# Kernel optimization log

Hardware: AMD Instinct MI355X
Metric: run time of the kernel (lower is better)

## Reference

```python
import jax, jax.numpy as jnp
import numpy as np

B, T, N, DG = 4, 24, 2048, 64
E, H, W, P, NH = 128, 64, 64, 8, 4
HD = E // NH
HP, WP = H // P, W // P
NP = HP * WP
SCALE = float(np.sqrt(HD))


def _mlp(x, w1, b1, w2, b2):
    return jax.nn.relu(x @ w1 + b1) @ w2 + b2


def _interp_linear(x, out_len):
    # x: (B, L, C); linear interpolation along L to out_len, align_corners=False (PyTorch semantics)
    L = x.shape[1]
    src = jnp.maximum((jnp.arange(out_len, dtype=jnp.float32) + 0.5) * (L / out_len) - 0.5, 0.0)
    i0 = jnp.floor(src).astype(jnp.int32)
    lam = (src - i0.astype(jnp.float32))[None, :, None]
    i1 = jnp.minimum(i0 + 1, L - 1)
    return x[:, i0] * (1.0 - lam) + x[:, i1] * lam


def _cross_attn(Q, K, V, qw, qb, kw, kb, vw, vb, ow, ob):
    b, ql, _ = Q.shape
    kl = K.shape[1]
    q = (Q @ qw + qb).reshape(b, ql, NH, HD).transpose(0, 2, 1, 3)
    k = (K @ kw + kb).reshape(b, kl, NH, HD).transpose(0, 2, 1, 3)
    v = (V @ vw + vb).reshape(b, kl, NH, HD).transpose(0, 2, 1, 3)
    s = jnp.einsum('bhqd,bhkd->bhqk', q, k) / SCALE
    a = jax.nn.softmax(s, axis=-1)
    o = jnp.einsum('bhqk,bhkd->bhqd', a, v).transpose(0, 2, 1, 3).reshape(b, ql, E)
    o = o @ ow + ob
    # permute -> F.interpolate(size=k_len, mode='linear') -> permute back
    return _interp_linear(o, kl)


def _forward(graph_features, grid_features, graph_time_indices, grid_time_indices,
             gek_w1, gek_b1, gek_w2, gek_b2, gev_w1, gev_b1, gev_w2, gev_b2,
             rk_w1, rk_b1, rk_w2, rk_b2, rv_w1, rv_b1, rv_w2, rv_b2,
             te_w1, te_b1, te_w2, te_b2, pe_w, pe_b, up_w, up_b,
             ag_q_w, ag_q_b, ag_k_w, ag_k_b, ag_v_w, ag_v_b, ag_o_w, ag_o_b,
             ar_q_w, ar_q_b, ar_k_w, ar_k_b, ar_v_w, ar_v_b, ar_o_w, ar_o_b):
    # time embedding (query), q_len = T
    te = _mlp(graph_time_indices[:, :, None], te_w1, te_b1, te_w2, te_b2)  # (B, T, E)
    # graph branch
    gf = graph_features.reshape(B, T * N, DG)
    gk = _mlp(gf, gek_w1, gek_b1, gek_w2, gek_b2)
    gv = _mlp(gf, gev_w1, gev_b1, gev_w2, gev_b2)
    g_out = _cross_attn(te, gk, gv, ag_q_w, ag_q_b, ag_k_w, ag_k_b, ag_v_w, ag_v_b, ag_o_w, ag_o_b)
    g_out = g_out.reshape(B, T, N, E)
    # grid branch: non-overlapping patch conv (kernel=stride=P) as einsum
    xp = grid_features.reshape(B * T, E, HP, P, WP, P)
    patches = jnp.einsum('bchpwq,ocpq->bhwo', xp, pe_w) + pe_b  # (BT, HP, WP, E)
    patches = patches.reshape(B, T * NP, E)
    rk = _mlp(patches, rk_w1, rk_b1, rk_w2, rk_b2)
    rv = _mlp(patches, rv_w1, rv_b1, rv_w2, rv_b2)
    r_out = _cross_attn(te, rk, rv, ar_q_w, ar_q_b, ar_k_w, ar_k_b, ar_v_w, ar_v_b, ar_o_w, ar_o_b)  # (B, T*NP, E)
    r = r_out.reshape(B * T, HP, WP, E)
    # ConvTranspose2d with kernel=stride=P: each pixel expands to a PxP block
    up = jnp.einsum('bijc,copq->boipjq', r, up_w).reshape(B * T, E, H, W) + up_b[None, :, None, None]
    return g_out, up.reshape(B, T, E, H, W)


def setup_inputs():
    key = jax.random.key(0)
    ks = iter(jax.random.split(key, 64))
    def mk(shape):
        return jax.random.normal(next(ks), shape, dtype=jnp.float32) * 0.02
    d = {}
    d['graph_features'] = jax.random.normal(next(ks), (B, T, N, DG), dtype=jnp.float32)
    d['grid_features'] = jax.random.normal(next(ks), (B, T, E, H, W), dtype=jnp.float32)
    d['graph_time_indices'] = jax.random.uniform(next(ks), (B, T), dtype=jnp.float32)
    d['grid_time_indices'] = jax.random.uniform(next(ks), (B, T), dtype=jnp.float32)
    for pfx, din in (('gek', DG), ('gev', DG), ('rk', E), ('rv', E), ('te', 1)):
        d[pfx + '_w1'] = mk((din, E)); d[pfx + '_b1'] = jnp.zeros((E,), jnp.float32)
        d[pfx + '_w2'] = mk((E, E)); d[pfx + '_b2'] = jnp.zeros((E,), jnp.float32)
    d['pe_w'] = mk((E, E, P, P)); d['pe_b'] = jnp.zeros((E,), jnp.float32)
    d['up_w'] = mk((E, E, P, P)); d['up_b'] = jnp.zeros((E,), jnp.float32)
    for pfx in ('ag', 'ar'):
        for nm in ('q', 'k', 'v', 'o'):
            d[pfx + '_' + nm + '_w'] = mk((E, E)); d[pfx + '_' + nm + '_b'] = jnp.zeros((E,), jnp.float32)
    return d


def reference(graph_features, grid_features, graph_time_indices, grid_time_indices,
              gek_w1, gek_b1, gek_w2, gek_b2, gev_w1, gev_b1, gev_w2, gev_b2,
              rk_w1, rk_b1, rk_w2, rk_b2, rv_w1, rv_b1, rv_w2, rv_b2,
              te_w1, te_b1, te_w2, te_b2, pe_w, pe_b, up_w, up_b,
              ag_q_w, ag_q_b, ag_k_w, ag_k_b, ag_v_w, ag_v_b, ag_o_w, ag_o_b,
              ar_q_w, ar_q_b, ar_k_w, ar_k_b, ar_v_w, ar_v_b, ar_o_w, ar_o_b):
    return _forward(graph_features, grid_features, graph_time_indices, grid_time_indices,
                    gek_w1, gek_b1, gek_w2, gek_b2, gev_w1, gev_b1, gev_w2, gev_b2,
                    rk_w1, rk_b1, rk_w2, rk_b2, rv_w1, rv_b1, rv_w2, rv_b2,
                    te_w1, te_b1, te_w2, te_b2, pe_w, pe_b, up_w, up_b,
                    ag_q_w, ag_q_b, ag_k_w, ag_k_b, ag_v_w, ag_v_b, ag_o_w, ag_o_b,
                    ar_q_w, ar_q_b, ar_k_w, ar_k_b, ar_v_w, ar_v_b, ar_o_w, ar_o_b)
```

## Files before the change

### kernel.cpp

```cpp
#include <hip/hip_runtime.h>


typedef unsigned short u16;
using bf8 = __attribute__((ext_vector_type(8))) short;
using f4v = __attribute__((ext_vector_type(4))) float;
#define MFMA16(a, b, c) __builtin_amdgcn_mfma_f32_16x16x32_bf16(a, b, c, 0, 0, 0)

constexpr float INV_SCALE = 0.17677669529663687f;

__device__ __forceinline__ u16 f2bf(float f) {
  unsigned u = __float_as_uint(f);
  u += 0x7FFFu + ((u >> 16) & 1u);
  return (u16)(u >> 16);
}
__device__ __forceinline__ unsigned pk2(float a, float b) {
  return (unsigned)f2bf(a) | ((unsigned)f2bf(b) << 16);
}
__device__ __forceinline__ float bflo(unsigned v) { return __uint_as_float(v << 16); }
__device__ __forceinline__ float bfhi(unsigned v) { return __uint_as_float(v & 0xffff0000u); }


__global__ __launch_bounds__(128) void k_pre1(
    const float* gk_w1, const float* gv_w1, const float* rk_w1, const float* rv_w1,
    u16* W1c_g, u16* W1c_r,
    const float* pe_w, u16* peB,
    const float* tidx, const float* te_w1, const float* te_b1,
    const float* te_w2, const float* te_b2,
    const float* wg, const float* bg, const float* wr, const float* br,
    float* qg, float* qr,
    const float* A0, const float* Ab0, const float* B0, const float* Bb0, float* O0, float* Ob0,
    const float* A1, const float* Ab1, const float* B1, const float* Bb1, float* O1, float* Ob1,
    const float* A2, const float* Ab2, const float* B2, const float* Bb2, float* O2, float* Ob2,
    const float* A3, const float* Ab3, const float* B3, const float* Bb3, float* O3, float* Ob3) {
  int x = blockIdx.x, e = threadIdx.x;
  __shared__ float sh[256];
  if (x < 512) {
    int c = x & 255, brn = x >> 8;
    int DIN = brn ? 128 : 64;
    if (e < DIN) {
      const float* src = brn ? (c < 128 ? rk_w1 : rv_w1) : (c < 128 ? gk_w1 : gv_w1);
      u16* dst = brn ? W1c_r : W1c_g;
      dst[c * DIN + e] = f2bf(src[e * 128 + (c & 127)]);
    }
  } else if (x < 1536) {
    int i = ((x - 512) * 128 + e) * 8;
    float4 v0 = *(const float4*)(pe_w + i);
    float4 v1 = *(const float4*)(pe_w + i + 4);
    uint4 o; o.x = pk2(v0.x, v0.y); o.y = pk2(v0.z, v0.w);
    o.z = pk2(v1.x, v1.y); o.w = pk2(v1.z, v1.w);
    *(uint4*)&peB[i] = o;
  } else if (x < 1632) {
    int row = x - 1536;
    float tv = tidx[row];
    sh[e] = fmaxf(tv * te_w1[e] + te_b1[e], 0.f);
    __syncthreads();
    float a = te_b2[e];
    for (int j = 0; j < 128; ++j) a += sh[j] * te_w2[j * 128 + e];
    sh[128 + e] = a;
    __syncthreads();
    float ag = bg[e], ar = br[e];
    for (int j = 0; j < 128; ++j) {
      float xx = sh[128 + j];
      ag += xx * wg[j * 128 + e];
      ar += xx * wr[j * 128 + e];
    }
    qg[row * 128 + e] = ag;
    qr[row * 128 + e] = ar;
  } else {
    int sub = x - 1632;
    int task = sub / 129, j = sub % 129;
    const float *A, *Ab, *Bm, *Bb; float *O, *Ob;
    switch (task) {
      case 0: A=A0; Ab=Ab0; Bm=B0; Bb=Bb0; O=O0; Ob=Ob0; break;
      case 1: A=A1; Ab=Ab1; Bm=B1; Bb=Bb1; O=O1; Ob=Ob1; break;
      case 2: A=A2; Ab=Ab2; Bm=B2; Bb=Bb2; O=O2; Ob=Ob2; break;
      default:A=A3; Ab=Ab3; Bm=B3; Bb=Bb3; O=O3; Ob=Ob3; break;
    }
    sh[e] = (j < 128) ? A[j * 128 + e] : Ab[e];
    __syncthreads();
    float acc = (j < 128) ? 0.f : Bb[e];
    for (int m = 0; m < 128; ++m) acc += sh[m] * Bm[m * 128 + e];
    if (j < 128) O[j * 128 + e] = acc; else Ob[e] = acc;
  }
}


__global__ __launch_bounds__(128) void k_wvopk(
    const float* Wv_g, const float* bv_g, const float* ow_g, const float* ob_g, float* Wvo_g, float* bvo_g,
    const float* Wv_r, const float* bv_r, const float* ow_r, const float* ob_r, float* Wvo_r, float* bvo_r,
    const float* Wk_g, const float* bk_g, const float* q_g, u16* PkT_g, float* ck_g,
    const float* Wk_r, const float* bk_r, const float* q_r, u16* PkT_r, float* ck_r) {
  int j = blockIdx.x, e = threadIdx.x;
  if (blockIdx.y < 8) {
    int br = blockIdx.y >> 2, h = blockIdx.y & 3;
    const float* Wv = br ? Wv_r : Wv_g;  const float* bv = br ? bv_r : bv_g;
    const float* ow = br ? ow_r : ow_g;  const float* ob = br ? ob_r : ob_g;
    float* Wvo = br ? Wvo_r : Wvo_g;     float* bvo = br ? bvo_r : bvo_g;
    if (j < 128) {
      __shared__ float wrow[32];
      if (e < 32) wrow[e] = Wv[j * 128 + h * 32 + e];
      __syncthreads();
      float acc = 0.f;
      for (int d = 0; d < 32; ++d) acc += wrow[d] * ow[(h * 32 + d) * 128 + e];
      Wvo[(h * 128 + j) * 128 + e] = acc;
    } else if (h == 0) {
      __shared__ float bbv[128];
      bbv[e] = bv[e];
      __syncthreads();
      float acc = ob[e];
      for (int m = 0; m < 128; ++m) acc += bbv[m] * ow[m * 128 + e];
      bvo[e] = acc;
    }
  } else {
    int y = blockIdx.y - 8;
    int br = y >> 2, b = y & 3;
    int hq = e;
    if (hq >= 96) return;
    const float* Wk = br ? Wk_r : Wk_g;  const float* bk = br ? bk_r : bk_g;
    const float* q  = br ? q_r  : q_g;
    u16* PkT = br ? PkT_r : PkT_g;       float* ck = br ? ck_r : ck_g;
    int h = hq / 24, t = hq % 24;
    const float* qrow = q + (b * 24 + t) * 128 + h * 32;
    if (j < 128) {
      const float* wrow = Wk + j * 128 + h * 32;
      float acc = 0.f;
      for (int d = 0; d < 32; ++d) acc += wrow[d] * qrow[d];
      PkT[((size_t)b * 96 + hq) * 136 + j] = f2bf(acc * INV_SCALE);
    } else {
      float acc = 0.f;
      for (int d = 0; d < 32; ++d) acc += bk[h * 32 + d] * qrow[d];
      ck[b * 96 + hq] = acc * INV_SCALE;
    }
  }
}


template <int DIN, int NRED, bool INBF>
__device__ __forceinline__ void flash_body(char* smem,
    const void* __restrict__ Xv, const float* __restrict__ redbias, size_t rstride,
    const u16* __restrict__ W1c, const float* __restrict__ b1k, const float* __restrict__ b1v,
    const u16* __restrict__ PkT, const float* __restrict__ ck,
    u16* __restrict__ accP, float* __restrict__ lP,
    int KL, int kpb, int chunk, int b, int nchunk) {
  constexpr int KS = DIN / 32;
  constexpr int PD = DIN + 8;
  constexpr int PH = 136, PV = 72, PP = 72;
  constexpr int NR = DIN / 16;
  constexpr int XTN = 64 * PD;
  u16* Xt   = (u16*)smem;
  u16* HB   = (u16*)(smem + 4 * XTN);
  u16* Pt   = (u16*)(smem + 4 * XTN + 18432);
  u16* Pk_s = (u16*)(smem + 4 * XTN + 18432 + 13824);
  float* lred = (float*)(smem + 4 * XTN + 18432 + 13824 + 26112);

  int t = threadIdx.x;
  int l = t & 63, w = t >> 6;
  int l16 = l & 15, l4 = l >> 4;

  size_t xbase = (size_t)b * KL * DIN + (size_t)chunk * kpb * DIN;

  {
    const unsigned* ps = (const unsigned*)(PkT + (size_t)b * 96 * 136);
    unsigned* pd = (unsigned*)Pk_s;
    for (int i = t; i < 96 * 136 / 2; i += 256) pd[i] = ps[i];
  }

  bf8 wkA[2][KS], wvB[2][KS];
#pragma unroll
  for (int m = 0; m < 2; ++m)
#pragma unroll
    for (int ks = 0; ks < KS; ++ks) {
      int hid = w * 32 + m * 16 + l16;
      wkA[m][ks] = *(const bf8*)(W1c + (size_t)hid * DIN + ks * 32 + l4 * 8);
      wvB[m][ks] = *(const bf8*)(W1c + (size_t)(128 + hid) * DIN + ks * 32 + l4 * 8);
    }
  float bkA[2][4], bvB[2], ckr[6];
#pragma unroll
  for (int m = 0; m < 2; ++m)
#pragma unroll
    for (int r = 0; r < 4; ++r) bkA[m][r] = b1k[w * 32 + m * 16 + l4 * 4 + r];
#pragma unroll
  for (int n = 0; n < 2; ++n) bvB[n] = b1v[w * 32 + n * 16 + l16];
#pragma unroll
  for (int n = 0; n < 6; ++n) ckr[n] = ck[b * 96 + n * 16 + l16];

  f4v accO[6][2];
#pragma unroll
  for (int m = 0; m < 6; ++m)
#pragma unroll
    for (int n = 0; n < 2; ++n) accO[m][n] = (f4v){0.f, 0.f, 0.f, 0.f};
  float lacc[6] = {0.f, 0.f, 0.f, 0.f, 0.f, 0.f};

  float4 xr[NR];
  auto load_tile = [&](int kt) {
#pragma unroll
    for (int r = 0; r < NR; ++r) {
      int idx = (r * 256 + t) * 4;
      if constexpr (!INBF) {
        const float* Xrow = (const float*)Xv + xbase + (size_t)kt * 64 * DIN;
        xr[r] = *(const float4*)(Xrow + idx);
      } else {
        const u16* Xrow = (const u16*)Xv + xbase + (size_t)kt * 64 * DIN;
        int din = idx % DIN;
        float4 a = *(const float4*)(redbias + din);
#pragma unroll
        for (int c = 0; c < NRED; ++c) {
          uint2 v = *(const uint2*)(Xrow + (size_t)c * rstride + idx);
          a.x += bflo(v.x); a.y += bfhi(v.x);
          a.z += bflo(v.y); a.w += bfhi(v.y);
        }
        xr[r] = a;
      }
    }
  };

  int ntile = kpb >> 6;
  load_tile(0);
  int buf = 0;
  for (int kt = 0; kt < ntile; ++kt) {
#pragma unroll
    for (int r = 0; r < NR; ++r) {
      int idx = (r * 256 + t) * 4;
      int key = idx / DIN, din = idx % DIN;
      uint2 o; o.x = pk2(xr[r].x, xr[r].y); o.y = pk2(xr[r].z, xr[r].w);
      *(uint2*)&Xt[buf * XTN + key * PD + din] = o;
    }
    if (kt + 1 < ntile) load_tile(kt + 1);
    __syncthreads();

    {
      f4v hk[2][4];
#pragma unroll
      for (int m = 0; m < 2; ++m)
#pragma unroll
        for (int n = 0; n < 4; ++n) hk[m][n] = (f4v){0.f, 0.f, 0.f, 0.f};
#pragma unroll
      for (int ks = 0; ks < KS; ++ks) {
        bf8 xf[4];
#pragma unroll
        for (int n = 0; n < 4; ++n)
          xf[n] = *(const bf8*)&Xt[buf * XTN + (n * 16 + l16) * PD + ks * 32 + l4 * 8];
#pragma unroll
        for (int m = 0; m < 2; ++m)
#pragma unroll
          for (int n = 0; n < 4; ++n) hk[m][n] = MFMA16(wkA[m][ks], xf[n], hk[m][n]);
      }
#pragma unroll
      for (int m = 0; m < 2; ++m)
#pragma unroll
        for (int n = 0; n < 4; ++n) {
          int key = n * 16 + l16;
          int hid0 = w * 32 + m * 16 + l4 * 4;
          float v0 = fmaxf(hk[m][n][0] + bkA[m][0], 0.f);
          float v1 = fmaxf(hk[m][n][1] + bkA[m][1], 0.f);
          float v2 = fmaxf(hk[m][n][2] + bkA[m][2], 0.f);
          float v3 = fmaxf(hk[m][n][3] + bkA[m][3], 0.f);
          uint2 o; o.x = pk2(v0, v1); o.y = pk2(v2, v3);
          *(uint2*)&HB[key * PH + hid0] = o;
        }
    }
    __syncthreads();

    {
      f4v sa[6];
#pragma unroll
      for (int n = 0; n < 6; ++n) sa[n] = (f4v){ckr[n], ckr[n], ckr[n], ckr[n]};
#pragma unroll
      for (int ks = 0; ks < 4; ++ks) {
        bf8 a = *(const bf8*)&HB[(w * 16 + l16) * PH + ks * 32 + l4 * 8];
#pragma unroll
        for (int n = 0; n < 6; ++n) {
          bf8 bp = *(const bf8*)&Pk_s[(n * 16 + l16) * 136 + ks * 32 + l4 * 8];
          sa[n] = MFMA16(a, bp, sa[n]);
        }
      }
#pragma unroll
      for (int n = 0; n < 6; ++n) {
        float e0 = __expf(sa[n][0]), e1 = __expf(sa[n][1]);
        float e2 = __expf(sa[n][2]), e3 = __expf(sa[n][3]);
        float ls = (e0 + e1) + (e2 + e3);
        ls += __shfl_xor(ls, 16);
        ls += __shfl_xor(ls, 32);
        lacc[n] += ls;
        uint2 o; o.x = pk2(e0, e1); o.y = pk2(e2, e3);
        *(uint2*)&Pt[(n * 16 + l16) * PP + w * 16 + l4 * 4] = o;
      }
    }
    __syncthreads();

    {
      f4v hv[4][2];
#pragma unroll
      for (int m = 0; m < 4; ++m)
#pragma unroll
        for (int n = 0; n < 2; ++n) hv[m][n] = (f4v){0.f, 0.f, 0.f, 0.f};
#pragma unroll
      for (int ks = 0; ks < KS; ++ks) {
        bf8 xa[4];
#pragma unroll
        for (int m = 0; m < 4; ++m)
          xa[m] = *(const bf8*)&Xt[buf * XTN + (m * 16 + l16) * PD + ks * 32 + l4 * 8];
#pragma unroll
        for (int m = 0; m < 4; ++m)
#pragma unroll
          for (int n = 0; n < 2; ++n) hv[m][n] = MFMA16(xa[m], wvB[n][ks], hv[m][n]);
      }
#pragma unroll
      for (int m = 0; m < 4; ++m)
#pragma unroll
        for (int n = 0; n < 2; ++n) {
          int d = w * 32 + n * 16 + l16;
          int key0 = m * 16 + l4 * 4;
          float v0 = fmaxf(hv[m][n][0] + bvB[n], 0.f);
          float v1 = fmaxf(hv[m][n][1] + bvB[n], 0.f);
          float v2 = fmaxf(hv[m][n][2] + bvB[n], 0.f);
          float v3 = fmaxf(hv[m][n][3] + bvB[n], 0.f);
          uint2 o; o.x = pk2(v0, v1); o.y = pk2(v2, v3);
          *(uint2*)&HB[d * PV + key0] = o;
        }
    }

#pragma unroll
    for (int ks = 0; ks < 2; ++ks) {
      bf8 pa[6];
#pragma unroll
      for (int m = 0; m < 6; ++m)
        pa[m] = *(const bf8*)&Pt[(m * 16 + l16) * PP + ks * 32 + l4 * 8];
#pragma unroll
      for (int n = 0; n < 2; ++n) {
        bf8 hb = *(const bf8*)&HB[(w * 32 + n * 16 + l16) * PV + ks * 32 + l4 * 8];
#pragma unroll
        for (int m = 0; m < 6; ++m) accO[m][n] = MFMA16(pa[m], hb, accO[m][n]);
      }
    }
    buf ^= 1;
  }

  u16* ap = accP + (size_t)(b * nchunk + chunk) * 96 * 128;
#pragma unroll
  for (int m = 0; m < 6; ++m)
#pragma unroll
    for (int n = 0; n < 2; ++n) {
      int d = w * 32 + n * 16 + l16;
#pragma unroll
      for (int r = 0; r < 4; ++r) {
        int hq = m * 16 + l4 * 4 + r;
        ap[hq * 128 + d] = f2bf(accO[m][n][r]);
      }
    }
  if (l4 == 0) {
#pragma unroll
    for (int n = 0; n < 6; ++n) lred[w * 96 + n * 16 + l16] = lacc[n];
  }
  __syncthreads();
  if (t < 96) {
    float s = lred[t] + lred[96 + t] + lred[192 + t] + lred[288 + t];
    lP[(size_t)(b * nchunk + chunk) * 96 + t] = s;
  }
}


__device__ __forceinline__ void patch_body(char* smem, int bt, int kc,
    const float* __restrict__ X, const u16* __restrict__ peB,
    u16* __restrict__ patchP) {
  u16* Xp = (u16*)smem;
  u16* Wt = (u16*)(smem + 17408);
  int t = threadIdx.x;
  int l = t & 63, w = t >> 6;
  int l16 = l & 15, l4 = l >> 4;
  const float* Xbt = X + (size_t)bt * 524288 + (size_t)kc * 65536;

  f4v acc[4][2];
#pragma unroll
  for (int m = 0; m < 4; ++m)
#pragma unroll
    for (int n = 0; n < 2; ++n) acc[m][n] = (f4v){0.f, 0.f, 0.f, 0.f};

  float4 xr[8];
  auto loadX = [&](int s) {
    const float* img = Xbt + (size_t)s * 8192;
#pragma unroll
    for (int r = 0; r < 8; ++r) xr[r] = *(const float4*)(img + (r * 256 + t) * 4);
  };
  loadX(0);

  for (int s = 0; s < 8; ++s) {
#pragma unroll
    for (int r = 0; r < 8; ++r) {
      int idx = (r * 256 + t) * 4;
      int cl = idx >> 12, off = idx & 4095;
      int h = off >> 6, w0 = off & 63;
      int patch = (h >> 3) * 8 + (w0 >> 3);
      int within = (h & 7) * 8 + (w0 & 7);
      uint2 o; o.x = pk2(xr[r].x, xr[r].y); o.y = pk2(xr[r].z, xr[r].w);
      *(uint2*)&Xp[patch * 136 + cl * 64 + within] = o;
    }
    {
      int colbase = kc * 1024 + s * 128;
#pragma unroll
      for (int r = 0; r < 8; ++r) {
        int idx = r * 256 + t;
        int co = idx >> 4, part = idx & 15;
        int slot = part ^ (co & 7);
        uint4 v = *(const uint4*)(peB + (size_t)co * 8192 + colbase + part * 8);
        *(uint4*)&Wt[co * 128 + slot * 8] = v;
      }
    }
    if (s < 7) loadX(s + 1);
    __syncthreads();
#pragma unroll
    for (int ks2 = 0; ks2 < 4; ++ks2) {
      bf8 af[4];
#pragma unroll
      for (int m = 0; m < 4; ++m)
        af[m] = *(const bf8*)&Xp[(m * 16 + l16) * 136 + ks2 * 32 + l4 * 8];
#pragma unroll
      for (int n = 0; n < 2; ++n) {
        int co = w * 32 + n * 16 + l16;
        int slot = (ks2 * 4 + l4) ^ (co & 7);
        bf8 bf_ = *(const bf8*)&Wt[co * 128 + slot * 8];
#pragma unroll
        for (int m = 0; m < 4; ++m) acc[m][n] = MFMA16(af[m], bf_, acc[m][n]);
      }
    }
    __syncthreads();
  }
  u16* outp = patchP + ((size_t)kc * 6144 + bt * 64) * 128;
#pragma unroll
  for (int m = 0; m < 4; ++m)
#pragma unroll
    for (int n = 0; n < 2; ++n) {
      int d = w * 32 + n * 16 + l16;
#pragma unroll
      for (int r = 0; r < 4; ++r) {
        int patch = m * 16 + l4 * 4 + r;
        outp[patch * 128 + d] = f2bf(acc[m][n][r]);
      }
    }
}


__device__ __forceinline__ void ogred_body(char* smem, int t, int b, int nc,
    const u16* __restrict__ accP, const float* __restrict__ lP,
    const float* __restrict__ Wvo, const float* __restrict__ bvo,
    float* __restrict__ og) {
  float* part = (float*)smem;
  float* invl = part + 2048;
  float* red  = part + 2052;
  int tid = threadIdx.x;
  int oct = tid & 15, h = (tid >> 4) & 3, cq = tid >> 6;
  int cn = nc >> 2;
  float a8[8];
#pragma unroll
  for (int k = 0; k < 8; ++k) a8[k] = 0.f;
  const u16* base = accP + ((size_t)(b * nc + cq * cn) * 96 + h * 24 + t) * 128 + oct * 8;
  for (int c = 0; c < cn; ++c) {
    uint4 v = *(const uint4*)(base + (size_t)c * 12288);
    a8[0] += bflo(v.x); a8[1] += bfhi(v.x);
    a8[2] += bflo(v.y); a8[3] += bfhi(v.y);
    a8[4] += bflo(v.z); a8[5] += bfhi(v.z);
    a8[6] += bflo(v.w); a8[7] += bfhi(v.w);
  }
#pragma unroll
  for (int k = 0; k < 8; ++k) part[cq * 512 + h * 128 + oct * 8 + k] = a8[k];
  if (tid < 64) {
    int hh = tid >> 4, c0 = tid & 15;
    float ls = 0.f;
    for (int c = c0; c < nc; c += 16) ls += lP[(size_t)(b * nc + c) * 96 + hh * 24 + t];
    ls += __shfl_xor(ls, 8); ls += __shfl_xor(ls, 4);
    ls += __shfl_xor(ls, 2); ls += __shfl_xor(ls, 1);
    if (c0 == 0) invl[hh] = 1.f / ls;
  }
  __syncthreads();
  for (int p = tid; p < 512; p += 256) {
    float s = (part[p] + part[512 + p]) + (part[1024 + p] + part[1536 + p]);
    part[p] = s * invl[p >> 7];
  }
  __syncthreads();
  {
    int e = tid & 127, jh = tid >> 7;
    float acc = jh ? 0.f : bvo[e];
    for (int h2 = 0; h2 < 4; ++h2) {
      const float* wv = Wvo + (size_t)(h2 * 128 + jh * 64) * 128 + e;
      const float* o = part + h2 * 128 + jh * 64;
#pragma unroll 4
      for (int j = 0; j < 64; ++j) acc += o[j] * wv[(size_t)j * 128];
    }
    red[tid] = acc;
  }
  __syncthreads();
  if (tid < 128) og[(b * 24 + t) * 128 + tid] = red[tid] + red[128 + tid];
}


__global__ __launch_bounds__(256, 2) void k_big1(
    const float* __restrict__ gf, const u16* __restrict__ W1c_g,
    const float* __restrict__ gek_b1, const float* __restrict__ gev_b1,
    const u16* __restrict__ PkT_g, const float* __restrict__ ck_g,
    u16* __restrict__ accP_g, float* __restrict__ lP_g,
    const float* __restrict__ gridf, const u16* __restrict__ peB,
    u16* __restrict__ patchP) {
  __shared__ __align__(16) char smem[78336];
  int x = blockIdx.x;
  int r5 = x % 5, q5 = x / 5;
  if (r5 < 2) {
    int fid = q5 * 2 + r5;
    flash_body<64, 1, false>(smem, gf, (const float*)nullptr, 0,
        W1c_g, gek_b1, gev_b1, PkT_g, ck_g, accP_g, lP_g,
        49152, 384, fid & 127, fid >> 7, 128);
  } else {
    int pid = q5 * 3 + (r5 - 2);
    patch_body(smem, pid % 96, pid / 96, gridf, peB, patchP);
  }
}


__global__ __launch_bounds__(256, 2) void k_big2(
    const u16* __restrict__ accP_g, const float* __restrict__ lP_g,
    const float* __restrict__ Wvo_g, const float* __restrict__ bvo_g,
    float* __restrict__ og_g,
    const u16* __restrict__ patchP, const float* __restrict__ pe_b,
    const u16* __restrict__ W1c_r,
    const float* __restrict__ rk_b1, const float* __restrict__ rv_b1,
    const u16* __restrict__ PkT_r, const float* __restrict__ ck_r,
    u16* __restrict__ accP_r, float* __restrict__ lP_r) {
  __shared__ __align__(16) char smem[94720];
  int x = blockIdx.x;
  int id = x >> 1;
  if (x & 1) {
    flash_body<128, 8, true>(smem, patchP, pe_b, 786432,
        W1c_r, rk_b1, rv_b1, PkT_r, ck_r, accP_r, lP_r,
        1536, 64, id % 24, id / 24, 24);
  } else {
    ogred_body(smem, id % 24, id / 24, 128, accP_g, lP_g, Wvo_g, bvo_g, og_g);
  }
}


__global__ __launch_bounds__(256) void k_ogr(
    const u16* __restrict__ accP_r, const float* __restrict__ lP_r,
    const float* __restrict__ Wvo_r, const float* __restrict__ bvo_r,
    float* __restrict__ og_r) {
  __shared__ __align__(16) char smem[9232];
  int x = blockIdx.x;
  ogred_body(smem, x % 24, x / 24, 24, accP_r, lP_r, Wvo_r, bvo_r, og_r);
}


__global__ __launch_bounds__(256) void k_writers(const float* __restrict__ og_r,
    const float* __restrict__ up_w, const float* __restrict__ up_b,
    float* __restrict__ outu,
    const float* __restrict__ og_g, float* __restrict__ outg) {
  __shared__ float og_s[24 * 128];
  __shared__ float upw_s[128 * 64];
  __shared__ float U_s[24 * 64];
  int x = blockIdx.x;
  if (x < 512) {
    int b = x >> 7, o = x & 127;
    int tid = threadIdx.x;
    for (int i = tid; i < 24 * 128 / 4; i += 256)
      ((float4*)og_s)[i] = ((const float4*)(og_r + b * 3072))[i];
    for (int i = tid; i < 128 * 64 / 4; i += 256) {
      int c = i >> 4, pq4 = i & 15;
      ((float4*)upw_s)[i] = *(const float4*)(up_w + (size_t)c * 8192 + o * 64 + pq4 * 4);
    }
    __syncthreads();
    float bias = up_b[o];
    int pq = tid & 63, tg = tid >> 6;
    float acc[6] = {0.f, 0.f, 0.f, 0.f, 0.f, 0.f};
    for (int c = 0; c < 128; c += 4) {
      float w0 = upw_s[c * 64 + pq], w1 = upw_s[(c + 1) * 64 + pq];
      float w2 = upw_s[(c + 2) * 64 + pq], w3 = upw_s[(c + 3) * 64 + pq];
#pragma unroll
      for (int r = 0; r < 6; ++r) {
        float4 g = *(const float4*)&og_s[(tg * 6 + r) * 128 + c];
        acc[r] += g.x * w0 + g.y * w1 + g.z * w2 + g.w * w3;
      }
    }
#pragma unroll
    for (int r = 0; r < 6; ++r) U_s[(tg * 6 + r) * 64 + pq] = acc[r] + bias;
    __syncthreads();
    for (int i4 = tid; i4 < 24 * 1024; i4 += 256) {
      int i = i4 * 4;
      int t = i >> 12, hw = i & 4095;
      int h = hw >> 6, w0 = hw & 63;
      int ii = h >> 3, p = h & 7, j = w0 >> 3, q0 = w0 & 7;
      int n = t * 64 + ii * 8 + j;
      float src = fmaxf((n + 0.5f) * (1.f / 64.f) - 0.5f, 0.f);
      int t0 = (int)src; float lam = src - (float)t0; int t1 = min(t0 + 1, 23);
      float4 a = *(const float4*)&U_s[t0 * 64 + p * 8 + q0];
      float4 c4 = *(const float4*)&U_s[t1 * 64 + p * 8 + q0];
      float4 r;
      r.x = a.x + lam * (c4.x - a.x); r.y = a.y + lam * (c4.y - a.y);
      r.z = a.z + lam * (c4.z - a.z); r.w = a.w + lam * (c4.w - a.w);
      *(float4*)&outu[((size_t)(b * 24 + t) * 128 + o) * 4096 + hw] = r;
    }
  } else {
    int vx = x - 512;
    int b = vx >> 10;
    const float* ogb = og_g + b * 3072;
    float* ob = outg + (size_t)b * 6291456;
    for (int i4 = (vx & 1023) * 256 + threadIdx.x; i4 < 1572864; i4 += 1024 * 256) {
      int i = i4 * 4;
      int n = i >> 7, e = i & 127;
      float src = fmaxf((n + 0.5f) * (1.f / 2048.f) - 0.5f, 0.f);
      int t0 = (int)src; float lam = src - (float)t0; int t1 = min(t0 + 1, 23);
      float4 a = *(const float4*)&ogb[t0 * 128 + e];
      float4 c = *(const float4*)&ogb[t1 * 128 + e];
      float4 o;
      o.x = a.x + lam * (c.x - a.x); o.y = a.y + lam * (c.y - a.y);
      o.z = a.z + lam * (c.z - a.z); o.w = a.w + lam * (c.w - a.w);
      *(float4*)&ob[i] = o;
    }
  }
}


extern "C" void kernel_launch(void* const* d_in, const int* in_sizes, int n_in,
                              void* d_out, int out_size, void* d_ws, size_t ws_size,
                              hipStream_t stream) {
  (void)in_sizes; (void)n_in; (void)out_size; (void)ws_size;
  const float* gf    = (const float*)d_in[0];
  const float* gridf = (const float*)d_in[1];
  const float* gti   = (const float*)d_in[2];
  const float* gek_w1 = (const float*)d_in[4],  *gek_b1 = (const float*)d_in[5];
  const float* gek_w2 = (const float*)d_in[6],  *gek_b2 = (const float*)d_in[7];
  const float* gev_w1 = (const float*)d_in[8],  *gev_b1 = (const float*)d_in[9];
  const float* gev_w2 = (const float*)d_in[10], *gev_b2 = (const float*)d_in[11];
  const float* rk_w1  = (const float*)d_in[12], *rk_b1  = (const float*)d_in[13];
  const float* rk_w2  = (const float*)d_in[14], *rk_b2  = (const float*)d_in[15];
  const float* rv_w1  = (const float*)d_in[16], *rv_b1  = (const float*)d_in[17];
  const float* rv_w2  = (const float*)d_in[18], *rv_b2  = (const float*)d_in[19];
  const float* te_w1  = (const float*)d_in[20], *te_b1  = (const float*)d_in[21];
  const float* te_w2  = (const float*)d_in[22], *te_b2  = (const float*)d_in[23];
  const float* pe_w   = (const float*)d_in[24], *pe_b   = (const float*)d_in[25];
  const float* up_w   = (const float*)d_in[26], *up_b   = (const float*)d_in[27];
  const float* ag_q_w = (const float*)d_in[28], *ag_q_b = (const float*)d_in[29];
  const float* ag_k_w = (const float*)d_in[30], *ag_k_b = (const float*)d_in[31];
  const float* ag_v_w = (const float*)d_in[32], *ag_v_b = (const float*)d_in[33];
  const float* ag_o_w = (const float*)d_in[34], *ag_o_b = (const float*)d_in[35];
  const float* ar_q_w = (const float*)d_in[36], *ar_q_b = (const float*)d_in[37];
  const float* ar_k_w = (const float*)d_in[38], *ar_k_b = (const float*)d_in[39];
  const float* ar_v_w = (const float*)d_in[40], *ar_v_b = (const float*)d_in[41];
  const float* ar_o_w = (const float*)d_in[42], *ar_o_b = (const float*)d_in[43];

  float* out = (float*)d_out;
  float* ws = (float*)d_ws;
  size_t off = 0;
  auto A = [&](size_t n) { float* p = ws + off; off += n; return p; };
  float* q_g   = A(12288);   float* q_r   = A(12288);
  float* Wk_g  = A(16384);   float* bk_g  = A(128);
  float* Wv_g  = A(16384);   float* bv_g  = A(128);
  float* Wk_r  = A(16384);   float* bk_r  = A(128);
  float* Wv_r  = A(16384);   float* bv_r  = A(128);
  float* Wvo_g = A(65536);   float* bvo_g = A(128);
  float* Wvo_r = A(65536);   float* bvo_r = A(128);
  float* ck_g  = A(384);     float* ck_r  = A(384);
  u16*   PkT_g = (u16*)A(26112);
  u16*   PkT_r = (u16*)A(26112);
  u16*   W1c_g = (u16*)A(8192);
  u16*   W1c_r = (u16*)A(16384);
  u16*   peB   = (u16*)A(524288);
  float* lP_g  = A(49152);   float* lP_r  = A(9216);
  float* og_g  = A(12288);   float* og_r  = A(12288);
  u16*   accP_g = (u16*)A(3145728);
  u16*   patchP = (u16*)A(3145728);
  u16*   accP_r = (u16*)A(589824);

  k_pre1<<<2148, 128, 0, stream>>>(
      gek_w1, gev_w1, rk_w1, rv_w1, W1c_g, W1c_r,
      pe_w, peB,
      gti, te_w1, te_b1, te_w2, te_b2, ag_q_w, ag_q_b, ar_q_w, ar_q_b, q_g, q_r,
      gek_w2, gek_b2, ag_k_w, ag_k_b, Wk_g, bk_g,
      gev_w2, gev_b2, ag_v_w, ag_v_b, Wv_g, bv_g,
      rk_w2,  rk_b2,  ar_k_w, ar_k_b, Wk_r, bk_r,
      rv_w2,  rv_b2,  ar_v_w, ar_v_b, Wv_r, bv_r);
  k_wvopk<<<dim3(129, 16), 128, 0, stream>>>(
      Wv_g, bv_g, ag_o_w, ag_o_b, Wvo_g, bvo_g,
      Wv_r, bv_r, ar_o_w, ar_o_b, Wvo_r, bvo_r,
      Wk_g, bk_g, q_g, PkT_g, ck_g,
      Wk_r, bk_r, q_r, PkT_r, ck_r);

  k_big1<<<1280, 256, 0, stream>>>(
      gf, W1c_g, gek_b1, gev_b1, PkT_g, ck_g, accP_g, lP_g,
      gridf, peB, patchP);
  k_big2<<<192, 256, 0, stream>>>(
      accP_g, lP_g, Wvo_g, bvo_g, og_g,
      patchP, pe_b, W1c_r, rk_b1, rv_b1, PkT_r, ck_r, accP_r, lP_r);
  k_ogr<<<96, 256, 0, stream>>>(accP_r, lP_r, Wvo_r, bvo_r, og_r);
  k_writers<<<4608, 256, 0, stream>>>(og_r, up_w, up_b, out + 25165824, og_g, out);
}
```

Before: 213.5 us.

## Rebalance flash split counts and move graph broadcast writer alongside grid reduction

Reduces the number of key-chunk splits in both flash-attention stages: 32 instead of 128 for the graph branch and 8 instead of 24 for the grid branch. This shrinks the partial-accumulator buffers and the split-reduction work in ogred. Block interleaving in k_big1/k_big2 becomes contiguous ranges. The graph-output broadcast writer now shares a launch with the grid split reduction, overlapping it with the reduction instead of waiting behind it, and the up-projection writer becomes its own kernel. Fewer, longer flash blocks reduce merge overhead but may lower occupancy and load balance across CUs.

```diff
diff --git a/kernel.cpp b/kernel.cpp
--- a/kernel.cpp
+++ b/kernel.cpp
@@ -502,14 +502,12 @@
     u16* __restrict__ patchP) {
   __shared__ __align__(16) char smem[78336];
   int x = blockIdx.x;
-  int r5 = x % 5, q5 = x / 5;
-  if (r5 < 2) {
-    int fid = q5 * 2 + r5;
+  if (x < 128) {
     flash_body<64, 1, false>(smem, gf, (const float*)nullptr, 0,
         W1c_g, gek_b1, gev_b1, PkT_g, ck_g, accP_g, lP_g,
-        49152, 384, fid & 127, fid >> 7, 128);
+        49152, 1536, x & 31, x >> 5, 32);
   } else {
-    int pid = q5 * 3 + (r5 - 2);
+    int pid = x - 128;
     patch_body(smem, pid % 96, pid / 96, gridf, peB, patchP);
   }
 }
@@ -526,77 +524,28 @@
     u16* __restrict__ accP_r, float* __restrict__ lP_r) {
   __shared__ __align__(16) char smem[94720];
   int x = blockIdx.x;
-  int id = x >> 1;
-  if (x & 1) {
+  if (x < 96) {
+    ogred_body(smem, x % 24, x / 24, 32, accP_g, lP_g, Wvo_g, bvo_g, og_g);
+  } else {
+    int fid = x - 96;
     flash_body<128, 8, true>(smem, patchP, pe_b, 786432,
         W1c_r, rk_b1, rv_b1, PkT_r, ck_r, accP_r, lP_r,
-        1536, 64, id % 24, id / 24, 24);
-  } else {
-    ogred_body(smem, id % 24, id / 24, 128, accP_g, lP_g, Wvo_g, bvo_g, og_g);
-  }
-}
-
-
-__global__ __launch_bounds__(256) void k_ogr(
+        1536, 192, fid & 7, fid >> 3, 8);
+  }
+}
+
+
+__global__ __launch_bounds__(256) void k_big3(
     const u16* __restrict__ accP_r, const float* __restrict__ lP_r,
     const float* __restrict__ Wvo_r, const float* __restrict__ bvo_r,
-    float* __restrict__ og_r) {
+    float* __restrict__ og_r,
+    const float* __restrict__ og_g, float* __restrict__ outg) {
   __shared__ __align__(16) char smem[9232];
   int x = blockIdx.x;
-  ogred_body(smem, x % 24, x / 24, 24, accP_r, lP_r, Wvo_r, bvo_r, og_r);
-}
-
-
-__global__ __launch_bounds__(256) void k_writers(const float* __restrict__ og_r,
-    const float* __restrict__ up_w, const float* __restrict__ up_b,
-    float* __restrict__ outu,
-    const float* __restrict__ og_g, float* __restrict__ outg) {
-  __shared__ float og_s[24 * 128];
-  __shared__ float upw_s[128 * 64];
-  __shared__ float U_s[24 * 64];
-  int x = blockIdx.x;
-  if (x < 512) {
-    int b = x >> 7, o = x & 127;
-    int tid = threadIdx.x;
-    for (int i = tid; i < 24 * 128 / 4; i += 256)
-      ((float4*)og_s)[i] = ((const float4*)(og_r + b * 3072))[i];
-    for (int i = tid; i < 128 * 64 / 4; i += 256) {
-      int c = i >> 4, pq4 = i & 15;
-      ((float4*)upw_s)[i] = *(const float4*)(up_w + (size_t)c * 8192 + o * 64 + pq4 * 4);
-    }
-    __syncthreads();
-    float bias = up_b[o];
-    int pq = tid & 63, tg = tid >> 6;
-    float acc[6] = {0.f, 0.f, 0.f, 0.f, 0.f, 0.f};
-    for (int c = 0; c < 128; c += 4) {
-      float w0 = upw_s[c * 64 + pq], w1 = upw_s[(c + 1) * 64 + pq];
-      float w2 = upw_s[(c + 2) * 64 + pq], w3 = upw_s[(c + 3) * 64 + pq];
-#pragma unroll
-      for (int r = 0; r < 6; ++r) {
-        float4 g = *(const float4*)&og_s[(tg * 6 + r) * 128 + c];
-        acc[r] += g.x * w0 + g.y * w1 + g.z * w2 + g.w * w3;
-      }
-    }
-#pragma unroll
-    for (int r = 0; r < 6; ++r) U_s[(tg * 6 + r) * 64 + pq] = acc[r] + bias;
-    __syncthreads();
-    for (int i4 = tid; i4 < 24 * 1024; i4 += 256) {
-      int i = i4 * 4;
-      int t = i >> 12, hw = i & 4095;
-      int h = hw >> 6, w0 = hw & 63;
-      int ii = h >> 3, p = h & 7, j = w0 >> 3, q0 = w0 & 7;
-      int n = t * 64 + ii * 8 + j;
-      float src = fmaxf((n + 0.5f) * (1.f / 64.f) - 0.5f, 0.f);
-      int t0 = (int)src; float lam = src - (float)t0; int t1 = min(t0 + 1, 23);
-      float4 a = *(const float4*)&U_s[t0 * 64 + p * 8 + q0];
-      float4 c4 = *(const float4*)&U_s[t1 * 64 + p * 8 + q0];
-      float4 r;
-      r.x = a.x + lam * (c4.x - a.x); r.y = a.y + lam * (c4.y - a.y);
-      r.z = a.z + lam * (c4.z - a.z); r.w = a.w + lam * (c4.w - a.w);
-      *(float4*)&outu[((size_t)(b * 24 + t) * 128 + o) * 4096 + hw] = r;
-    }
+  if (x < 96) {
+    ogred_body(smem, x % 24, x / 24, 8, accP_r, lP_r, Wvo_r, bvo_r, og_r);
   } else {
-    int vx = x - 512;
+    int vx = x - 96;
     int b = vx >> 10;
     const float* ogb = og_g + b * 3072;
     float* ob = outg + (size_t)b * 6291456;
@@ -612,6 +561,54 @@
       o.z = a.z + lam * (c.z - a.z); o.w = a.w + lam * (c.w - a.w);
       *(float4*)&ob[i] = o;
     }
+  }
+}
+
+
+__global__ __launch_bounds__(256) void k_upfuse(const float* __restrict__ og_r,
+    const float* __restrict__ up_w, const float* __restrict__ up_b,
+    float* __restrict__ outu) {
+  int b = blockIdx.x >> 7, o = blockIdx.x & 127;
+  __shared__ float og_s[24 * 128];
+  __shared__ float upw_s[128 * 64];
+  __shared__ float U_s[24 * 64];
+  int tid = threadIdx.x;
+  for (int i = tid; i < 24 * 128 / 4; i += 256)
+    ((float4*)og_s)[i] = ((const float4*)(og_r + b * 3072))[i];
+  for (int i = tid; i < 128 * 64 / 4; i += 256) {
+    int c = i >> 4, pq4 = i & 15;
+    ((float4*)upw_s)[i] = *(const float4*)(up_w + (size_t)c * 8192 + o * 64 + pq4 * 4);
+  }
+  __syncthreads();
+  float bias = up_b[o];
+  int pq = tid & 63, tg = tid >> 6;
+  float acc[6] = {0.f, 0.f, 0.f, 0.f, 0.f, 0.f};
+  for (int c = 0; c < 128; c += 4) {
+    float w0 = upw_s[c * 64 + pq], w1 = upw_s[(c + 1) * 64 + pq];
+    float w2 = upw_s[(c + 2) * 64 + pq], w3 = upw_s[(c + 3) * 64 + pq];
+#pragma unroll
+    for (int r = 0; r < 6; ++r) {
+      float4 g = *(const float4*)&og_s[(tg * 6 + r) * 128 + c];
+      acc[r] += g.x * w0 + g.y * w1 + g.z * w2 + g.w * w3;
+    }
+  }
+#pragma unroll
+  for (int r = 0; r < 6; ++r) U_s[(tg * 6 + r) * 64 + pq] = acc[r] + bias;
+  __syncthreads();
+  for (int i4 = tid; i4 < 24 * 1024; i4 += 256) {
+    int i = i4 * 4;
+    int t = i >> 12, hw = i & 4095;
+    int h = hw >> 6, w0 = hw & 63;
+    int ii = h >> 3, p = h & 7, j = w0 >> 3, q0 = w0 & 7;
+    int n = t * 64 + ii * 8 + j;
+    float src = fmaxf((n + 0.5f) * (1.f / 64.f) - 0.5f, 0.f);
+    int t0 = (int)src; float lam = src - (float)t0; int t1 = min(t0 + 1, 23);
+    float4 a = *(const float4*)&U_s[t0 * 64 + p * 8 + q0];
+    float4 c4 = *(const float4*)&U_s[t1 * 64 + p * 8 + q0];
+    float4 r;
+    r.x = a.x + lam * (c4.x - a.x); r.y = a.y + lam * (c4.y - a.y);
+    r.z = a.z + lam * (c4.z - a.z); r.w = a.w + lam * (c4.w - a.w);
+    *(float4*)&outu[((size_t)(b * 24 + t) * 128 + o) * 4096 + hw] = r;
   }
 }
 
@@ -661,11 +658,11 @@
   u16*   W1c_g = (u16*)A(8192);
   u16*   W1c_r = (u16*)A(16384);
   u16*   peB   = (u16*)A(524288);
-  float* lP_g  = A(49152);   float* lP_r  = A(9216);
+  float* lP_g  = A(12288);   float* lP_r  = A(3072);
   float* og_g  = A(12288);   float* og_r  = A(12288);
-  u16*   accP_g = (u16*)A(3145728);
+  u16*   accP_g = (u16*)A(786432);
   u16*   patchP = (u16*)A(3145728);
-  u16*   accP_r = (u16*)A(589824);
+  u16*   accP_r = (u16*)A(196608);
 
   k_pre1<<<2148, 128, 0, stream>>>(
       gek_w1, gev_w1, rk_w1, rv_w1, W1c_g, W1c_r,
@@ -681,12 +678,13 @@
       Wk_g, bk_g, q_g, PkT_g, ck_g,
       Wk_r, bk_r, q_r, PkT_r, ck_r);
 
-  k_big1<<<1280, 256, 0, stream>>>(
+  k_big1<<<896, 256, 0, stream>>>(
       gf, W1c_g, gek_b1, gev_b1, PkT_g, ck_g, accP_g, lP_g,
       gridf, peB, patchP);
-  k_big2<<<192, 256, 0, stream>>>(
+  k_big2<<<128, 256, 0, stream>>>(
       accP_g, lP_g, Wvo_g, bvo_g, og_g,
       patchP, pe_b, W1c_r, rk_b1, rv_b1, PkT_r, ck_r, accP_r, lP_r);
-  k_ogr<<<96, 256, 0, stream>>>(accP_r, lP_r, Wvo_r, bvo_r, og_r);
-  k_writers<<<4608, 256, 0, stream>>>(og_r, up_w, up_b, out + 25165824, og_g, out);
-}
+  k_big3<<<4192, 256, 0, stream>>>(
+      accP_r, lP_r, Wvo_r, bvo_r, og_r, og_g, out);
+  k_upfuse<<<512, 256, 0, stream>>>(og_r, up_w, up_b, out + 25165824);
+}
```

Result: faster. 206.2 us (-3.4%).
